# Kernel optimization log

Hardware: AMD Instinct MI355X
Metric: run time of the kernel (lower is better)

Reference implementation:

```python
import jax, jax.numpy as jnp
import numpy as np

K = 1024          # num_embeddings
D = 128           # embedding_dim
EMA_DECAY = 0.99
EPS = 1e-5


def setup_inputs() -> dict:
    key = jax.random.key(0)
    k1, k2, k3 = jax.random.split(key, 3)
    z = jax.random.normal(k1, (64, D, 32, 32), dtype=jnp.float32)
    codebook = jax.random.normal(k2, (K, D), dtype=jnp.float32)
    ema_count = jnp.zeros((K,), dtype=jnp.float32)
    ema_weight = jax.random.normal(k3, (K, D), dtype=jnp.float32)
    return {"z": z, "codebook": codebook, "ema_count": ema_count, "ema_weight": ema_weight}


def reference(z, codebook, ema_count, ema_weight):
    B, C, H, W = z.shape
    # flatten to [N, D] in BHWC order (matches permute(0,2,3,1).view(-1, D))
    z_flat = jnp.transpose(z, (0, 2, 3, 1)).reshape(-1, D)  # [N, D]

    # squared euclidean distances [N, K]
    distances = (
        jnp.sum(z_flat * z_flat, axis=1, keepdims=True)
        + jnp.sum(codebook * codebook, axis=1)
        - 2.0 * jnp.matmul(z_flat, codebook.T)
    )
    indices = jnp.argmin(distances, axis=1)  # [N] int

    # gather instead of one-hot @ codebook (same math)
    quantized_flat = codebook[indices]  # [N, D]
    # NOTE: faithful to original: raw view of BHWC-ordered flat buffer into z.shape
    quantized = quantized_flat.reshape(z.shape)

    # EMA statistics (no_grad in original): segment sums instead of one-hot matmuls
    encodings_sum = jax.ops.segment_sum(jnp.ones_like(indices, dtype=jnp.float32), indices, num_segments=K)
    dw = jax.ops.segment_sum(z_flat, indices, num_segments=K)  # [K, D]
    new_ema_count = EMA_DECAY * ema_count + (1.0 - EMA_DECAY) * encodings_sum
    new_ema_weight = EMA_DECAY * ema_weight + (1.0 - EMA_DECAY) * dw
    n = jnp.sum(new_ema_count)
    weights = (new_ema_count + EPS) / (n + K * EPS) * n
    new_codebook = new_ema_weight / weights[:, None]

    commitment_loss = jnp.mean((jax.lax.stop_gradient(quantized) - z) ** 2)
    codebook_loss = jnp.mean((quantized - jax.lax.stop_gradient(z)) ** 2)

    # straight-through estimator
    quantized_st = z + jax.lax.stop_gradient(quantized - z)

    idx_map = indices.reshape(B, H, W)
    return (quantized_st, idx_map, commitment_loss, codebook_loss,
            new_codebook, new_ema_count, new_ema_weight)
```

## Files before the change

### kernel.cpp

```cpp
#include <hip/hip_runtime.h>

#define NVEC 65536
#define KCB  1024
#define DIM  128
#define HW   1024
#define CHUNK 64
#define NCHUNKS (NVEC / CHUNK)

typedef __bf16 b16;
typedef b16 b16x8 __attribute__((ext_vector_type(8)));
typedef float f32x16 __attribute__((ext_vector_type(16)));

static __device__ __forceinline__ unsigned short f2bf(float f) {
  unsigned int x = __float_as_uint(f);
  unsigned int r = x + 0x7fffu + ((x >> 16) & 1u);
  return (unsigned short)(r >> 16);
}

__global__ void k_prep(const float* __restrict__ cb, const float* __restrict__ emw,
                       uint4* __restrict__ cbt, float* __restrict__ ccb,
                       double* __restrict__ cc64, float* __restrict__ out6,
                       int* __restrict__ hist) {
  const int t = blockIdx.x * blockDim.x + threadIdx.x;
  const int kc = t >> 11, u = t & 2047;
  const int code7 = u & 127, dch = u >> 7;
  const float* src = cb + (kc * 128 + code7) * 128 + dch * 8;
  const float4 x = *(const float4*)src;
  const float4 y = *(const float4*)(src + 4);
  uint4 o;
  o.x = (unsigned)f2bf(x.x) | ((unsigned)f2bf(x.y) << 16);
  o.y = (unsigned)f2bf(x.z) | ((unsigned)f2bf(x.w) << 16);
  o.z = (unsigned)f2bf(y.x) | ((unsigned)f2bf(y.y) << 16);
  o.w = (unsigned)f2bf(y.z) | ((unsigned)f2bf(y.w) << 16);
  cbt[t] = o;
  const float4 e0 = *(const float4*)(emw + (size_t)t * 8);
  const float4 e1 = *(const float4*)(emw + (size_t)t * 8 + 4);
  *(float2*)(out6 + (size_t)t * 8 + 0) = make_float2(0.99f * e0.x, 0.99f * e0.y);
  *(float2*)(out6 + (size_t)t * 8 + 2) = make_float2(0.99f * e0.z, 0.99f * e0.w);
  *(float2*)(out6 + (size_t)t * 8 + 4) = make_float2(0.99f * e1.x, 0.99f * e1.y);
  *(float2*)(out6 + (size_t)t * 8 + 6) = make_float2(0.99f * e1.z, 0.99f * e1.w);
  if (t < KCB) hist[t] = 0;
  if (blockIdx.x < 4) {
    const int k = blockIdx.x * 256 + threadIdx.x;
    const float* row = cb + k * DIM;
    double s = 0.0;
#pragma unroll 8
    for (int j = 0; j < DIM; ++j) {
      const double v = (double)row[j];
      s = fma(v, v, s);
    }
    cc64[k] = s;
    ccb[k] = 512.f - 0.5f * (float)s;
  }
}

__global__ __launch_bounds__(256, 4) void k_argmin6(
    const float* __restrict__ z, const uint4* __restrict__ cbt,
    const float* __restrict__ ccb, const double* __restrict__ cc64,
    const float* __restrict__ cb, float* __restrict__ z_t,
    float* __restrict__ out1, int* __restrict__ hist) {
  __shared__ __align__(16) float zs[128][65];
  __shared__ uint2 cand[64][2];
  uint4* Bs = (uint4*)zs;
  const int tid = threadIdx.x;
  const int l = tid & 63, wv = tid >> 6;
  const int g = l >> 5;
  const int lm = l & 31;
  const int wr = (wv & 1) * 32;
  const int wc = wv >> 1;
  const int n0 = blockIdx.x * 64;
  const int b = n0 >> 10;
  const int hwbase = n0 & (HW - 1);

  {
    const int hw4 = (tid & 15) * 4;
    const int dr = tid >> 4;
    const float* src = z + (size_t)b * 131072 + hwbase + hw4;
#pragma unroll
    for (int j = 0; j < 8; ++j) {
      const int d = dr + 16 * j;
      const float4 v = *(const float4*)(src + d * 1024);
      zs[d][hw4 + 0] = v.x; zs[d][hw4 + 1] = v.y;
      zs[d][hw4 + 2] = v.z; zs[d][hw4 + 3] = v.w;
    }
  }
  __syncthreads();

#pragma unroll
  for (int jj = 0; jj < 2; ++jj) {
    const int row = (tid >> 3) + 32 * jj;
    float* dst = z_t + ((size_t)(n0 + row)) * 128;
#pragma unroll
    for (int j = 0; j < 4; ++j) {
      const int d = (j * 8 + (tid & 7)) * 4;
      float4 v;
      v.x = zs[d + 0][row]; v.y = zs[d + 1][row];
      v.z = zs[d + 2][row]; v.w = zs[d + 3][row];
      *(float4*)(dst + d) = v;
    }
  }
  uint4 afrag[8];
  {
    const int row = wr + lm;
#pragma unroll
    for (int ks = 0; ks < 8; ++ks) {
      const int d0 = ks * 16 + g * 8;
      afrag[ks].x = (unsigned)f2bf(zs[d0 + 0][row]) | ((unsigned)f2bf(zs[d0 + 1][row]) << 16);
      afrag[ks].y = (unsigned)f2bf(zs[d0 + 2][row]) | ((unsigned)f2bf(zs[d0 + 3][row]) << 16);
      afrag[ks].z = (unsigned)f2bf(zs[d0 + 4][row]) | ((unsigned)f2bf(zs[d0 + 5][row]) << 16);
      afrag[ks].w = (unsigned)f2bf(zs[d0 + 6][row]) | ((unsigned)f2bf(zs[d0 + 7][row]) << 16);
    }
  }

  unsigned pm1[16], pm2[16];
#pragma unroll
  for (int r = 0; r < 16; ++r) { pm1[r] = 0u; pm2[r] = 0u; }

  for (int kc = 0; kc < 8; ++kc) {
    __syncthreads();
#pragma unroll
    for (int i = 0; i < 8; ++i) {
      __builtin_amdgcn_global_load_lds(&cbt[kc * 2048 + wv * 512 + i * 64 + l],
                                       &Bs[wv * 512 + i * 64], 16, 0, 0);
    }
    const float cv0 = ccb[kc * 128 + (wc * 2 + 0) * 32 + lm];
    const float cv1 = ccb[kc * 128 + (wc * 2 + 1) * 32 + lm];
    __syncthreads();

    f32x16 a0, a1;
#pragma unroll
    for (int j = 0; j < 16; ++j) { a0[j] = cv0; a1[j] = cv1; }
#pragma unroll
    for (int ks = 0; ks < 8; ++ks) {
      const b16x8 av = *reinterpret_cast<const b16x8*>(&afrag[ks]);
      const b16x8 bv0 = *reinterpret_cast<const b16x8*>(&Bs[(ks * 2 + g) * 128 + (wc * 2) * 32 + lm]);
      const b16x8 bv1 = *reinterpret_cast<const b16x8*>(&Bs[(ks * 2 + g) * 128 + (wc * 2 + 1) * 32 + lm]);
      a0 = __builtin_amdgcn_mfma_f32_32x32x16_bf16(av, bv0, a0, 0, 0, 0);
      a1 = __builtin_amdgcn_mfma_f32_32x32x16_bf16(av, bv1, a1, 0, 0, 0);
    }
    const unsigned ci0 = 1023u - (unsigned)(kc * 128 + (wc * 2) * 32 + lm);
    const unsigned ci1 = ci0 - 32u;
#pragma unroll
    for (int r = 0; r < 16; ++r) {
      {
        const unsigned uu = ((__float_as_uint(a0[r]) + 0x200u) & 0xFFFFFC00u) | ci0;
        const unsigned t = pm1[r] < uu ? pm1[r] : uu;
        pm1[r] = pm1[r] > uu ? pm1[r] : uu;
        pm2[r] = pm2[r] > t ? pm2[r] : t;
      }
      {
        const unsigned uu = ((__float_as_uint(a1[r]) + 0x200u) & 0xFFFFFC00u) | ci1;
        const unsigned t = pm1[r] < uu ? pm1[r] : uu;
        pm1[r] = pm1[r] > uu ? pm1[r] : uu;
        pm2[r] = pm2[r] > t ? pm2[r] : t;
      }
    }
  }

#pragma unroll
  for (int r = 0; r < 16; ++r) {
    unsigned u1 = pm1[r], u2 = pm2[r];
#pragma unroll
    for (int m = 1; m < 32; m <<= 1) {
      const unsigned o1 = (unsigned)__shfl_xor((int)u1, m, 64);
      const unsigned o2 = (unsigned)__shfl_xor((int)u2, m, 64);
      const unsigned s = u1 < o1 ? u1 : o1;
      u1 = u1 > o1 ? u1 : o1;
      u2 = u2 > o2 ? u2 : o2;
      u2 = u2 > s ? u2 : s;
    }
    if (lm == 0) {
      const int lrow = wr + (r & 3) + 8 * (r >> 2) + 4 * g;
      cand[lrow][wc] = make_uint2(u1, u2);
    }
  }
  __syncthreads();

  int* h = (int*)zs;
#pragma unroll
  for (int j = 0; j < 4; ++j) h[tid + 256 * j] = 0;
  __syncthreads();
  {
    const int row = tid >> 2, c = tid & 3;
    const uint2 cd = cand[row][c >> 1];
    const unsigned u = (c & 1) ? cd.y : cd.x;
    int k = 1023 - (int)(u & 1023u);
    const int n = n0 + row;
    const float4* zr = (const float4*)(z_t + (size_t)n * DIM);
    const float4* cr = (const float4*)(cb + k * DIM);
    double d = 0.0;
#pragma unroll 8
    for (int j = 0; j < DIM / 4; ++j) {
      const float4 zv = zr[j], cv = cr[j];
      d = fma((double)zv.x, (double)cv.x, d);
      d = fma((double)zv.y, (double)cv.y, d);
      d = fma((double)zv.z, (double)cv.z, d);
      d = fma((double)zv.w, (double)cv.w, d);
    }
    double s = fma(-2.0, d, cc64[k]);
#pragma unroll
    for (int m = 1; m < 4; m <<= 1) {
      const double os = __shfl_xor(s, m, 64);
      const int ok = __shfl_xor(k, m, 64);
      if (os < s || (os == s && ok < k)) { s = os; k = ok; }
    }
    if (c == 0) {
      out1[n] = (float)k;
      atomicAdd(&h[k], 1);
    }
  }
  __syncthreads();
#pragma unroll
  for (int j = 0; j < 4; ++j) {
    const int v = h[tid + 256 * j];
    if (v) atomicAdd(&hist[tid + 256 * j], v);
  }
}

__global__ void k_scan(const int* __restrict__ hist, const float* __restrict__ emc,
                       int* __restrict__ cursor, float* __restrict__ out5,
                       float* __restrict__ ntot) {
  __shared__ int tmp[KCB];
  __shared__ float red[16];
  const int t = threadIdx.x;
  const int v = hist[t];
  tmp[t] = v;
  __syncthreads();
  for (int off = 1; off < KCB; off <<= 1) {
    int x = 0;
    if (t >= off) x = tmp[t - off];
    __syncthreads();
    if (t >= off) tmp[t] += x;
    __syncthreads();
  }
  cursor[t] = tmp[t] - v;
  float o5 = 0.99f * emc[t] + 0.01f * (float)v;
  out5[t] = o5;
#pragma unroll
  for (int m = 32; m; m >>= 1) o5 += __shfl_xor(o5, m, 64);
  if ((t & 63) == 0) red[t >> 6] = o5;
  __syncthreads();
  if (t == 0) {
    float s = 0.f;
#pragma unroll
    for (int j = 0; j < 16; ++j) s += red[j];
    *ntot = s;
  }
}

__global__ void k_scatter(const float* __restrict__ idx_f, int* __restrict__ cursor,
                          int* __restrict__ order, int* __restrict__ key) {
  const int n = blockIdx.x * blockDim.x + threadIdx.x;
  const int k = (int)idx_f[n];
  const int pos = atomicAdd(&cursor[k], 1);
  order[pos] = n;
  key[pos] = k;
}

__global__ __launch_bounds__(128) void k_chunkreduce_q(
    float* zq, const float* __restrict__ cb,
    const int* __restrict__ order, const int* __restrict__ key,
    float* __restrict__ out6, float* __restrict__ lossp) {
  __shared__ int so[CHUNK], sk[CHUNK];
  __shared__ float red[2];
  const int t = threadIdx.x;
  const int base = blockIdx.x * CHUNK;
  if (t < CHUNK) { so[t] = order[base + t]; sk[t] = key[base + t]; }
  __syncthreads();
  int kprev = sk[0];
  float cbv = cb[kprev * 128 + t];
  float acc = 0.f, loss = 0.f;
  int i = 0;
  while (i < CHUNK) {
    if (i + 8 <= CHUNK && sk[i] == kprev && sk[i + 7] == kprev) {
      const int n0 = so[i + 0], n1 = so[i + 1], n2 = so[i + 2], n3 = so[i + 3];
      const int n4 = so[i + 4], n5 = so[i + 5], n6 = so[i + 6], n7 = so[i + 7];
      const float v0 = zq[(size_t)n0 * 128 + t];
      const float v1 = zq[(size_t)n1 * 128 + t];
      const float v2 = zq[(size_t)n2 * 128 + t];
      const float v3 = zq[(size_t)n3 * 128 + t];
      const float v4 = zq[(size_t)n4 * 128 + t];
      const float v5 = zq[(size_t)n5 * 128 + t];
      const float v6 = zq[(size_t)n6 * 128 + t];
      const float v7 = zq[(size_t)n7 * 128 + t];
      acc += ((v0 + v1) + (v2 + v3)) + ((v4 + v5) + (v6 + v7));
      float e;
      e = cbv - v0; loss = fmaf(e, e, loss);
      e = cbv - v1; loss = fmaf(e, e, loss);
      e = cbv - v2; loss = fmaf(e, e, loss);
      e = cbv - v3; loss = fmaf(e, e, loss);
      e = cbv - v4; loss = fmaf(e, e, loss);
      e = cbv - v5; loss = fmaf(e, e, loss);
      e = cbv - v6; loss = fmaf(e, e, loss);
      e = cbv - v7; loss = fmaf(e, e, loss);
      zq[(size_t)n0 * 128 + t] = cbv; zq[(size_t)n1 * 128 + t] = cbv;
      zq[(size_t)n2 * 128 + t] = cbv; zq[(size_t)n3 * 128 + t] = cbv;
      zq[(size_t)n4 * 128 + t] = cbv; zq[(size_t)n5 * 128 + t] = cbv;
      zq[(size_t)n6 * 128 + t] = cbv; zq[(size_t)n7 * 128 + t] = cbv;
      i += 8;
    } else {
      const int kk = sk[i];
      if (kk != kprev) {
        atomicAdd(&out6[kprev * 128 + t], 0.01f * acc);
        acc = 0.f; kprev = kk;
        cbv = cb[kk * 128 + t];
      }
      const int n = so[i];
      const float v = zq[(size_t)n * 128 + t];
      acc += v;
      const float e = cbv - v; loss = fmaf(e, e, loss);
      zq[(size_t)n * 128 + t] = cbv;
      ++i;
    }
  }
  atomicAdd(&out6[kprev * 128 + t], 0.01f * acc);
#pragma unroll
  for (int m = 32; m; m >>= 1) loss += __shfl_xor(loss, m, 64);
  if ((t & 63) == 0) red[t >> 6] = loss;
  __syncthreads();
  if (t == 0) lossp[blockIdx.x] = red[0] + red[1];
}

__global__ void k_final(const float* __restrict__ out5, const float* __restrict__ out6,
                        const float* __restrict__ ntot_p, const float* __restrict__ lossp,
                        float* __restrict__ out4, float* __restrict__ out2,
                        float* __restrict__ out3) {
  __shared__ float red[4];
  const int i = blockIdx.x * blockDim.x + threadIdx.x;
  const float ntot = *ntot_p;
  const int k = i >> 7;
  const float w = (out5[k] + 1e-5f) / (ntot + KCB * 1e-5f) * ntot;
  out4[i] = out6[i] / w;
  if (blockIdx.x == 511) {
    const int t = threadIdx.x;
    float s = 0.f;
#pragma unroll
    for (int j = 0; j < NCHUNKS / 256; ++j) s += lossp[t + 256 * j];
#pragma unroll
    for (int m = 32; m; m >>= 1) s += __shfl_xor(s, m, 64);
    if ((t & 63) == 0) red[t >> 6] = s;
    __syncthreads();
    if (t == 0) {
      const float lv = (red[0] + red[1] + red[2] + red[3]) * (1.f / 8388608.f);
      *out2 = lv; *out3 = lv;
    }
  }
}

extern "C" void kernel_launch(void* const* d_in, const int* in_sizes, int n_in,
                              void* d_out, int out_size, void* d_ws, size_t ws_size,
                              hipStream_t stream) {
  (void)in_sizes; (void)n_in; (void)out_size; (void)ws_size;
  const float* z   = (const float*)d_in[0];
  const float* cb  = (const float*)d_in[1];
  const float* emc = (const float*)d_in[2];
  const float* emw = (const float*)d_in[3];
  float* out = (float*)d_out;
  float* out0 = out;
  float* out1 = out + 8388608;
  float* out2 = out + 8454144;
  float* out3 = out + 8454145;
  float* out4 = out + 8454146;
  float* out5 = out + 8585218;
  float* out6 = out + 8586242;
  float* ws = (float*)d_ws;
  uint4* cbt      = (uint4*)ws;
  int* order      = (int*)(ws + 65536);
  int* key        = (int*)(ws + 131072);
  float* ccb      = ws + 327680;
  int* hist       = (int*)(ws + 328704);
  int* cursor     = (int*)(ws + 329728);
  float* ntot     = ws + 330752;
  float* lossp    = ws + 331776;
  double* cc64    = (double*)(ws + 333824);
  float* z_t = out0;

  hipLaunchKernelGGL(k_prep, dim3(64), dim3(256), 0, stream, cb, emw, cbt, ccb,
                     cc64, out6, hist);
  hipLaunchKernelGGL(k_argmin6, dim3(NVEC / 64), dim3(256), 0, stream,
                     z, cbt, ccb, cc64, cb, z_t, out1, hist);
  hipLaunchKernelGGL(k_scan, dim3(1), dim3(1024), 0, stream, hist, emc, cursor,
                     out5, ntot);
  hipLaunchKernelGGL(k_scatter, dim3(NVEC / 256), dim3(256), 0, stream, out1, cursor,
                     order, key);
  hipLaunchKernelGGL(k_chunkreduce_q, dim3(NCHUNKS), dim3(128), 0, stream,
                     z_t, cb, order, key, out6, lossp);
  hipLaunchKernelGGL(k_final, dim3(512), dim3(256), 0, stream, out5, out6, ntot,
                     lossp, out4, out2, out3);
}
```

Baseline: 129.8 us.

## Fold histogram scan into argmin via last-block pattern, pack order/key pairs

Removes the separate single-block scan launch. The last finishing argmin block, detected with a global done counter and threadfence, now computes the prefix sum, the EMA count update and the total count. The scatter now writes order and key as one packed uint2 instead of two separate int arrays, so the chunk reduction needs a single load per entry. This saves one kernel launch and the dependency bubble around it, at the cost of an extra global atomic per block and a serialized tail in one block.

```diff
diff --git a/kernel.cpp b/kernel.cpp
--- a/kernel.cpp
+++ b/kernel.cpp
@@ -20,7 +20,7 @@
 __global__ void k_prep(const float* __restrict__ cb, const float* __restrict__ emw,
                        uint4* __restrict__ cbt, float* __restrict__ ccb,
                        double* __restrict__ cc64, float* __restrict__ out6,
-                       int* __restrict__ hist) {
+                       int* __restrict__ hist, int* __restrict__ done) {
   const int t = blockIdx.x * blockDim.x + threadIdx.x;
   const int kc = t >> 11, u = t & 2047;
   const int code7 = u & 127, dch = u >> 7;
@@ -33,6 +33,7 @@
   o.z = (unsigned)f2bf(y.x) | ((unsigned)f2bf(y.y) << 16);
   o.w = (unsigned)f2bf(y.z) | ((unsigned)f2bf(y.w) << 16);
   cbt[t] = o;
+  if (t == 0) *done = 0;
   const float4 e0 = *(const float4*)(emw + (size_t)t * 8);
   const float4 e1 = *(const float4*)(emw + (size_t)t * 8 + 4);
   *(float2*)(out6 + (size_t)t * 8 + 0) = make_float2(0.99f * e0.x, 0.99f * e0.y);
@@ -57,10 +58,14 @@
 __global__ __launch_bounds__(256, 4) void k_argmin6(
     const float* __restrict__ z, const uint4* __restrict__ cbt,
     const float* __restrict__ ccb, const double* __restrict__ cc64,
-    const float* __restrict__ cb, float* __restrict__ z_t,
-    float* __restrict__ out1, int* __restrict__ hist) {
+    const float* __restrict__ cb, const float* __restrict__ emc,
+    float* __restrict__ z_t, float* __restrict__ out1, int* __restrict__ hist,
+    int* __restrict__ cursor, float* __restrict__ out5, float* __restrict__ ntot,
+    int* __restrict__ done) {
   __shared__ __align__(16) float zs[128][65];
   __shared__ uint2 cand[64][2];
+  __shared__ int isLast, wsum[4];
+  __shared__ float red[4];
   uint4* Bs = (uint4*)zs;
   const int tid = threadIdx.x;
   const int l = tid & 63, wv = tid >> 6;
@@ -215,57 +220,70 @@
     const int v = h[tid + 256 * j];
     if (v) atomicAdd(&hist[tid + 256 * j], v);
   }
-}
-
-__global__ void k_scan(const int* __restrict__ hist, const float* __restrict__ emc,
-                       int* __restrict__ cursor, float* __restrict__ out5,
-                       float* __restrict__ ntot) {
-  __shared__ int tmp[KCB];
-  __shared__ float red[16];
-  const int t = threadIdx.x;
-  const int v = hist[t];
-  tmp[t] = v;
-  __syncthreads();
-  for (int off = 1; off < KCB; off <<= 1) {
-    int x = 0;
-    if (t >= off) x = tmp[t - off];
+
+  __threadfence();
+  if (tid == 0) {
+    const int old = atomicAdd(done, 1);
+    isLast = (old == (int)gridDim.x - 1);
+  }
+  __syncthreads();
+  if (isLast) {
+    const int i0 = tid * 4;
+    const int v0 = atomicAdd(&hist[i0 + 0], 0);
+    const int v1 = atomicAdd(&hist[i0 + 1], 0);
+    const int v2 = atomicAdd(&hist[i0 + 2], 0);
+    const int v3 = atomicAdd(&hist[i0 + 3], 0);
+    const int ts = v0 + v1 + v2 + v3;
+    int x = ts;
+#pragma unroll
+    for (int dd = 1; dd < 64; dd <<= 1) {
+      const int y = __shfl_up(x, dd, 64);
+      if ((tid & 63) >= dd) x += y;
+    }
+    if ((tid & 63) == 63) wsum[tid >> 6] = x;
     __syncthreads();
-    if (t >= off) tmp[t] += x;
+    int wb = 0;
+#pragma unroll
+    for (int w = 0; w < 4; ++w) wb += (w < (tid >> 6)) ? wsum[w] : 0;
+    const int base = wb + x - ts;
+    cursor[i0 + 0] = base;
+    cursor[i0 + 1] = base + v0;
+    cursor[i0 + 2] = base + v0 + v1;
+    cursor[i0 + 3] = base + v0 + v1 + v2;
+    const float o0 = 0.99f * emc[i0 + 0] + 0.01f * (float)v0;
+    const float o1 = 0.99f * emc[i0 + 1] + 0.01f * (float)v1;
+    const float o2 = 0.99f * emc[i0 + 2] + 0.01f * (float)v2;
+    const float o3 = 0.99f * emc[i0 + 3] + 0.01f * (float)v3;
+    out5[i0 + 0] = o0; out5[i0 + 1] = o1;
+    out5[i0 + 2] = o2; out5[i0 + 3] = o3;
+    float p = o0 + o1 + o2 + o3;
+#pragma unroll
+    for (int m = 32; m; m >>= 1) p += __shfl_xor(p, m, 64);
+    if ((tid & 63) == 0) red[tid >> 6] = p;
     __syncthreads();
-  }
-  cursor[t] = tmp[t] - v;
-  float o5 = 0.99f * emc[t] + 0.01f * (float)v;
-  out5[t] = o5;
-#pragma unroll
-  for (int m = 32; m; m >>= 1) o5 += __shfl_xor(o5, m, 64);
-  if ((t & 63) == 0) red[t >> 6] = o5;
-  __syncthreads();
-  if (t == 0) {
-    float s = 0.f;
-#pragma unroll
-    for (int j = 0; j < 16; ++j) s += red[j];
-    *ntot = s;
+    if (tid == 0) *ntot = red[0] + red[1] + red[2] + red[3];
   }
 }
 
 __global__ void k_scatter(const float* __restrict__ idx_f, int* __restrict__ cursor,
-                          int* __restrict__ order, int* __restrict__ key) {
+                          uint2* __restrict__ ok) {
   const int n = blockIdx.x * blockDim.x + threadIdx.x;
   const int k = (int)idx_f[n];
   const int pos = atomicAdd(&cursor[k], 1);
-  order[pos] = n;
-  key[pos] = k;
+  ok[pos] = make_uint2((unsigned)n, (unsigned)k);
 }
 
 __global__ __launch_bounds__(128) void k_chunkreduce_q(
-    float* zq, const float* __restrict__ cb,
-    const int* __restrict__ order, const int* __restrict__ key,
+    float* zq, const float* __restrict__ cb, const uint2* __restrict__ ok,
     float* __restrict__ out6, float* __restrict__ lossp) {
   __shared__ int so[CHUNK], sk[CHUNK];
   __shared__ float red[2];
   const int t = threadIdx.x;
   const int base = blockIdx.x * CHUNK;
-  if (t < CHUNK) { so[t] = order[base + t]; sk[t] = key[base + t]; }
+  if (t < CHUNK) {
+    const uint2 v = ok[base + t];
+    so[t] = (int)v.x; sk[t] = (int)v.y;
+  }
   __syncthreads();
   int kprev = sk[0];
   float cbv = cb[kprev * 128 + t];
@@ -365,26 +383,25 @@
   float* out6 = out + 8586242;
   float* ws = (float*)d_ws;
   uint4* cbt      = (uint4*)ws;
-  int* order      = (int*)(ws + 65536);
-  int* key        = (int*)(ws + 131072);
+  uint2* okbuf    = (uint2*)(ws + 65536);
   float* ccb      = ws + 327680;
   int* hist       = (int*)(ws + 328704);
   int* cursor     = (int*)(ws + 329728);
   float* ntot     = ws + 330752;
+  int* done       = (int*)(ws + 330756);
   float* lossp    = ws + 331776;
   double* cc64    = (double*)(ws + 333824);
   float* z_t = out0;
 
   hipLaunchKernelGGL(k_prep, dim3(64), dim3(256), 0, stream, cb, emw, cbt, ccb,
-                     cc64, out6, hist);
+                     cc64, out6, hist, done);
   hipLaunchKernelGGL(k_argmin6, dim3(NVEC / 64), dim3(256), 0, stream,
-                     z, cbt, ccb, cc64, cb, z_t, out1, hist);
-  hipLaunchKernelGGL(k_scan, dim3(1), dim3(1024), 0, stream, hist, emc, cursor,
-                     out5, ntot);
+                     z, cbt, ccb, cc64, cb, emc, z_t, out1, hist, cursor,
+                     out5, ntot, done);
   hipLaunchKernelGGL(k_scatter, dim3(NVEC / 256), dim3(256), 0, stream, out1, cursor,
-                     order, key);
+                     okbuf);
   hipLaunchKernelGGL(k_chunkreduce_q, dim3(NCHUNKS), dim3(128), 0, stream,
-                     z_t, cb, order, key, out6, lossp);
+                     z_t, cb, okbuf, out6, lossp);
   hipLaunchKernelGGL(k_final, dim3(512), dim3(256), 0, stream, out5, out6, ntot,
                      lossp, out4, out2, out3);
 }
```

Measured after the change: 201.1 us. +55.0%, slower.
